# Kernel tuning notes

Measured on AMD Instinct MI355X. Metric: run time of the kernel, lower is better.

## Reference

```python
import jax, jax.numpy as jnp
import numpy as np

N_SUPPORT = 16384
EMBED_DIM = 1024
MAX_LEVELS = 4
N_CLASSES = 64


def setup_inputs() -> dict:
    key = jax.random.key(0)
    ks = jax.random.split(key, 12)
    D, L = EMBED_DIM, MAX_LEVELS
    s = 0.02
    return {
        "support_features": jax.random.normal(ks[0], (N_SUPPORT, D), jnp.float32),
        "support_labels": jax.random.randint(ks[1], (N_SUPPORT,), 0, N_CLASSES),
        "sp_w1": jax.random.normal(ks[2], (D, D // 2), jnp.float32) * s,
        "sp_b1": jnp.zeros((D // 2,), jnp.float32),
        "sp_w2": jax.random.normal(ks[3], (D // 2, L), jnp.float32) * s,
        "sp_b2": jnp.zeros((L,), jnp.float32),
        "lvl_emb": jax.random.normal(ks[4], (L, 1), jnp.float32) * s,
        "an_w1": jax.random.normal(ks[5], (L, D + 1, D), jnp.float32) * s,
        "an_b1": jnp.zeros((L, D), jnp.float32),
        "an_gamma": jnp.ones((L, D), jnp.float32),
        "an_beta": jnp.zeros((L, D), jnp.float32),
        "an_w2": jax.random.normal(ks[6], (L, D, D), jnp.float32) * s,
        "an_b2": jnp.zeros((L, D), jnp.float32),
        "fu_w1": jax.random.normal(ks[7], (L * D + L, D), jnp.float32) * s,
        "fu_b1": jnp.zeros((D,), jnp.float32),
        "fu_w2": jax.random.normal(ks[8], (D, D), jnp.float32) * s,
        "fu_b2": jnp.zeros((D,), jnp.float32),
        "n_classes": N_CLASSES,
    }


def _forward(support_features, support_labels, sp_w1, sp_b1, sp_w2, sp_b2,
             lvl_emb, an_w1, an_b1, an_gamma, an_beta, an_w2, an_b2,
             fu_w1, fu_b1, fu_w2, fu_b2, n_classes):
    N, D = support_features.shape
    L = an_w1.shape[0]
    # structure predictor on task context (mean pooled support set)
    task_context = support_features.mean(axis=0)
    h = jax.nn.relu(task_context @ sp_w1 + sp_b1)
    acts = jax.nn.sigmoid(h @ sp_w2 + sp_b2)  # [L]
    ones = jnp.ones((N,), support_features.dtype)
    counts = jax.ops.segment_sum(ones, support_labels, num_segments=n_classes)[:, None]
    counts = jnp.maximum(counts, 1.0)
    # per-level small MLP over ALL support points, then per-class mean via segment_sum
    protos = []
    for l in range(L):  # fixed small loop over structurally distinct level params
        xl = jnp.concatenate([support_features, jnp.broadcast_to(lvl_emb[l], (N, 1))], axis=1)  # [N, D+1]
        hh = xl @ an_w1[l] + an_b1[l]
        mu = hh.mean(axis=-1, keepdims=True)
        var = ((hh - mu) ** 2).mean(axis=-1, keepdims=True)
        hh = (hh - mu) / jnp.sqrt(var + 1e-5) * an_gamma[l] + an_beta[l]  # LayerNorm eps=1e-5
        hh = jax.nn.relu(hh)
        t = hh @ an_w2[l] + an_b2[l]
        protos.append(jax.ops.segment_sum(t, support_labels, num_segments=n_classes) / counts)
    protos = jnp.stack(protos, axis=1)  # [C, L, D]
    # data-dependent gating: pack prototypes of active levels (act > 0.1) to the front,
    # then active weights, then zero padding -- matching torch's concat+pad layout
    mask = acts > 0.1
    mi = mask.astype(jnp.int32)
    slots = jnp.cumsum(mi) - 1          # destination slot of each active level
    k = mi.sum()                        # number of active levels
    slot_or_dump = jnp.where(mask, slots, L)
    packed = jnp.zeros((n_classes, L + 1, D), protos.dtype).at[:, slot_or_dump, :].set(protos)[:, :L, :]
    S = L * D + L
    buf = jnp.zeros((n_classes, S + 1), protos.dtype)
    buf = buf.at[:, : L * D].set(packed.reshape(n_classes, L * D))
    widx = jnp.where(mask, k * D + slots, S)  # weights placed right after the k packed prototypes
    buf = buf.at[:, widx].set(jnp.broadcast_to(acts, (n_classes, L)))
    fusion_input = buf[:, :S]  # [C, L*D + L]
    fused = jax.nn.relu(fusion_input @ fu_w1 + fu_b1) @ fu_w2 + fu_b2  # [C, D]
    raw_mean = jax.ops.segment_sum(support_features, support_labels, num_segments=n_classes) / counts
    prototypes = jnp.where(k > 0, fused, raw_mean)
    level_contributions = jnp.where(mask, acts, 0.0)
    return prototypes, acts, level_contributions


def reference(support_features, support_labels, sp_w1, sp_b1, sp_w2, sp_b2,
              lvl_emb, an_w1, an_b1, an_gamma, an_beta, an_w2, an_b2,
              fu_w1, fu_b1, fu_w2, fu_b2, n_classes):
    return _forward(support_features, support_labels, sp_w1, sp_b1, sp_w2, sp_b2,
                    lvl_emb, an_w1, an_b1, an_gamma, an_beta, an_w2, an_b2,
                    fu_w1, fu_b1, fu_w2, fu_b2, n_classes)
```

## Files before the change

kernel.cpp:

```cpp
#include <hip/hip_runtime.h>
#include <hip/hip_bf16.h>
#include <stdint.h>

#define N_SUP 16384
#define DIM   1024
#define NLV   4
#define NCLS  64
#define NFUSE 4096

typedef __bf16 bf16x8 __attribute__((ext_vector_type(8)));
typedef __bf16 bf16x4 __attribute__((ext_vector_type(4)));
typedef float  f32x4  __attribute__((ext_vector_type(4)));

#define GLOAD_LDS16(g, l) \
    __builtin_amdgcn_global_load_lds((const __attribute__((address_space(1))) void*)(g), \
                                     (__attribute__((address_space(3))) void*)(l), 16, 0, 0)

__global__ __launch_bounds__(256) void k_count(const int* __restrict__ labels,
                                               int* __restrict__ gcnt) {
    __shared__ int hist[NCLS];
    int tid = threadIdx.x;
    if (tid < NCLS) hist[tid] = 0;
    __syncthreads();
    atomicAdd(&hist[labels[blockIdx.x * 256 + tid]], 1);
    __syncthreads();
    if (tid < NCLS && hist[tid] > 0) atomicAdd(&gcnt[tid], hist[tid]);
}

__global__ __launch_bounds__(64) void k_scan(const int* __restrict__ gcnt,
                                             int* __restrict__ gstart,
                                             int* __restrict__ gcur,
                                             float* __restrict__ counts_f) {
    int tid = threadIdx.x;
    __shared__ int s[NCLS];
    s[tid] = gcnt[tid];
    __syncthreads();
    if (tid == 0) {
        int run = 0;
        for (int c = 0; c < NCLS; ++c) { int v = s[c]; s[c] = run; run += v; }
    }
    __syncthreads();
    gstart[tid] = s[tid];
    gcur[tid] = s[tid];
    counts_f[tid] = fmaxf((float)gcnt[tid], 1.0f);
}

__global__ __launch_bounds__(256) void k_scatter(const int* __restrict__ labels,
                                                 int* __restrict__ gcur,
                                                 int* __restrict__ inv) {
    __shared__ int hist[NCLS];
    __shared__ int base[NCLS];
    int tid = threadIdx.x;
    int r = blockIdx.x * 256 + tid;
    if (tid < NCLS) hist[tid] = 0;
    __syncthreads();
    int lab = labels[r];
    int lrank = atomicAdd(&hist[lab], 1);
    __syncthreads();
    if (tid < NCLS && hist[tid] > 0) base[tid] = atomicAdd(&gcur[tid], hist[tid]);
    __syncthreads();
    inv[r] = base[lab] + lrank;
}

__global__ __launch_bounds__(256) void k_conv_feat(const float* __restrict__ f,
                                                   const int* __restrict__ inv,
                                                   __bf16* __restrict__ o) {
    int r = blockIdx.x;
    int tid = threadIdx.x;
    int dr = inv[r];
    float4 v = *(const float4*)(f + (size_t)r * DIM + tid * 4);
    union { __bf16 b[4]; uint64_t u; } pk;
    pk.b[0] = (__bf16)v.x; pk.b[1] = (__bf16)v.y;
    pk.b[2] = (__bf16)v.z; pk.b[3] = (__bf16)v.w;
    *(uint64_t*)(o + (size_t)dr * DIM + tid * 4) = pk.u;
}

__global__ __launch_bounds__(256) void k_wt(const float* __restrict__ an_w1,
                                            const float* __restrict__ an_b1,
                                            const float* __restrict__ lvl_emb,
                                            __bf16* __restrict__ w1t,
                                            float* __restrict__ eff) {
    __shared__ float tile[64][65];
    int m = blockIdx.z;
    const float* src = an_w1 + (size_t)m * 1025 * 1024;
    __bf16* dst = w1t + (size_t)m * 1024 * 1024;
    int k0 = blockIdx.x * 64, n0 = blockIdx.y * 64;
    int j = threadIdx.x & 63, i0 = threadIdx.x >> 6;
    #pragma unroll
    for (int ii = 0; ii < 16; ++ii) {
        int i = i0 + ii * 4;
        tile[i][j] = src[(size_t)(k0 + i) * 1024 + n0 + j];
    }
    __syncthreads();
    #pragma unroll
    for (int ii = 0; ii < 16; ++ii) {
        int i = i0 + ii * 4;
        dst[(size_t)(n0 + i) * 1024 + k0 + j] = (__bf16)tile[j][i];
    }
    if (blockIdx.y == 0 && threadIdx.x < 64) {
        int jj = k0 + threadIdx.x;
        eff[m * 1024 + jj] = an_b1[m * 1024 + jj]
                           + lvl_emb[m] * src[(size_t)1024 * 1024 + jj];
    }
}

__global__ __launch_bounds__(256) void k_gather(const __bf16* __restrict__ X,
                                                const int* __restrict__ gstart,
                                                const int* __restrict__ gcnt,
                                                float* __restrict__ outp,
                                                float* __restrict__ tcsum) {
    int c = blockIdx.x;
    int col = blockIdx.y * 256 + threadIdx.x;
    int st = gstart[c], n = gcnt[c];
    const __bf16* base = X + (size_t)st * DIM + col;
    float acc = 0.f;
    int i = 0;
    for (; i + 8 <= n; i += 8) {
        float v[8];
        #pragma unroll
        for (int j = 0; j < 8; ++j) v[j] = (float)base[(size_t)(i + j) * DIM];
        #pragma unroll
        for (int j = 0; j < 8; ++j) acc += v[j];
    }
    for (; i < n; ++i) acc += (float)base[(size_t)i * DIM];
    outp[(size_t)c * DIM + col] = acc;
    atomicAdd(&tcsum[col], acc);
}

__global__ __launch_bounds__(512) void k_gemv1(const float* __restrict__ tc,
                                               const float* __restrict__ sp_w1,
                                               float* __restrict__ hpre) {
    __shared__ float tcs[64];
    int tid = threadIdx.x;
    int kb = blockIdx.x * 64;
    if (tid < 64) tcs[tid] = tc[kb + tid] * (1.0f / N_SUP);
    __syncthreads();
    float acc = 0.f;
    #pragma unroll 8
    for (int k = 0; k < 64; ++k)
        acc += tcs[k] * sp_w1[(size_t)(kb + k) * 512 + tid];
    atomicAdd(&hpre[tid], acc);
}

__global__ __launch_bounds__(512) void k_head_fin(const float* __restrict__ hpre,
                                                  const float* __restrict__ sp_b1,
                                                  const float* __restrict__ sp_w2,
                                                  const float* __restrict__ sp_b2,
                                                  float* __restrict__ headf,
                                                  int* __restrict__ headi,
                                                  float* __restrict__ dout) {
    __shared__ float red[512];
    __shared__ float a4[4];
    int tid = threadIdx.x;
    float hv = hpre[tid] + sp_b1[tid];
    hv = hv > 0.f ? hv : 0.f;
    #pragma unroll
    for (int o = 0; o < 4; ++o) {
        red[tid] = hv * sp_w2[tid * 4 + o];
        __syncthreads();
        for (int st = 256; st > 0; st >>= 1) {
            if (tid < st) red[tid] += red[tid + st];
            __syncthreads();
        }
        if (tid == 0) a4[o] = 1.0f / (1.0f + expf(-(red[0] + sp_b2[o])));
        __syncthreads();
    }
    if (tid == 0) {
        int kk = 0;
        int lvl[4] = {-1, -1, -1, -1};
        for (int l = 0; l < 4; ++l)
            if (a4[l] > 0.1f) { lvl[kk] = l; kk++; }
        headi[0] = kk;
        for (int s = 0; s < 4; ++s) headi[1 + s] = lvl[s];
        for (int l = 0; l < 4; ++l) headf[l] = a4[l];
    }
    if (tid < 4) {
        dout[65536 + tid] = a4[tid];
        dout[65540 + tid] = a4[tid] > 0.1f ? a4[tid] : 0.f;
    }
}

__global__ __launch_bounds__(512, 2) void k_gemm256(const __bf16* __restrict__ A,
                                                    const __bf16* __restrict__ Bt,
                                                    const float* __restrict__ bias,
                                                    __bf16* __restrict__ C,
                                                    int K, int Nn, int NT) {
    __shared__ __bf16 lds[65536];
    const int tid = threadIdx.x;
    const int w   = tid >> 6;
    const int l   = tid & 63;
    const int wr  = w >> 2;
    const int wc  = w & 3;
    const int am  = l & 15;
    const int kg  = l >> 4;
    const size_t bm = (size_t)blockIdx.x * 256;
    const size_t bn = (size_t)blockIdx.y * 256;

    const int srow = w * 8 + (l >> 3);
    const int scol = ((l & 7) ^ (l >> 3)) * 8;
    const __bf16* gA[2][2]; const __bf16* gB[2][2];
    #pragma unroll
    for (int h = 0; h < 2; ++h)
        #pragma unroll
        for (int p = 0; p < 2; ++p) {
            gA[h][p] = A  + (bm + h * 128 + p * 64 + srow) * (size_t)K + scol;
            gB[h][p] = Bt + (bn + h * 128 + p * 64 + srow) * (size_t)K + scol;
        }

    f32x4 acc[8][4] = {};
    bf16x8 ax[4][2], ay[4][2], bx[2][2], by[2][2];

    #pragma unroll
    for (int h = 0; h < 2; ++h)
        #pragma unroll
        for (int p = 0; p < 2; ++p) {
            GLOAD_LDS16(gA[h][p], lds + h * 8192 + p * 4096 + w * 512);
            GLOAD_LDS16(gB[h][p], lds + 16384 + h * 8192 + p * 4096 + w * 512);
        }
    asm volatile("s_waitcnt vmcnt(0)" ::: "memory");
    __builtin_amdgcn_s_barrier();

    const int swzr = (am & 7) * 8;
    const int ko0 = (kg * 8) ^ swzr;
    const int ko1 = (32 + kg * 8) ^ swzr;
    {
        const __bf16* pa0 = lds + wr * 8192;
        #pragma unroll
        for (int i = 0; i < 4; ++i) {
            ax[i][0] = *(const bf16x8*)(pa0 + (i * 16 + am) * 64 + ko0);
            ax[i][1] = *(const bf16x8*)(pa0 + (i * 16 + am) * 64 + ko1);
        }
    }

#define MFMAQ(qm, qn, AF, BF) \
    __builtin_amdgcn_s_setprio(1); \
    _Pragma("unroll") \
    for (int i_ = 0; i_ < 4; ++i_) \
        _Pragma("unroll") \
        for (int j_ = 0; j_ < 2; ++j_) \
            _Pragma("unroll") \
            for (int k_ = 0; k_ < 2; ++k_) \
                acc[(qm) * 4 + i_][(qn) * 2 + j_] = __builtin_amdgcn_mfma_f32_16x16x32_bf16( \
                    AF[i_][k_], BF[j_][k_], acc[(qm) * 4 + i_][(qn) * 2 + j_], 0, 0, 0); \
    __builtin_amdgcn_s_setprio(0);

    for (int t = 0; t < NT; ++t) {
        const int cb = (t & 1) * 32768;
        const int nb = cb ^ 32768;
        const int tn = (t + 1) * 64;
        const bool more = (t + 1 < NT);
        const __bf16* pa  = lds + cb + wr * 8192;
        const __bf16* pan = lds + nb + wr * 8192;
        const __bf16* pb  = lds + cb + 16384 + (wc >> 1) * 8192 + (wc & 1) * 4096;

        if (more) {
            GLOAD_LDS16(gA[0][0] + tn, lds + nb + 0 * 4096 + w * 512);
            GLOAD_LDS16(gA[1][0] + tn, lds + nb + 8192 + 0 * 4096 + w * 512);
            asm volatile("s_waitcnt vmcnt(2)" ::: "memory");
        } else {
            asm volatile("s_waitcnt vmcnt(0)" ::: "memory");
        }
        __builtin_amdgcn_s_barrier();
        #pragma unroll
        for (int j = 0; j < 2; ++j) {
            bx[j][0] = *(const bf16x8*)(pb + (j * 16 + am) * 64 + ko0);
            bx[j][1] = *(const bf16x8*)(pb + (j * 16 + am) * 64 + ko1);
        }
        ay[0][0] = *(const bf16x8*)(pa + ((4 + 0) * 16 + am) * 64 + ko0);
        ay[0][1] = *(const bf16x8*)(pa + ((4 + 0) * 16 + am) * 64 + ko1);
        MFMAQ(0, 0, ax, bx)

        if (more) {
            GLOAD_LDS16(gA[0][1] + tn, lds + nb + 1 * 4096 + w * 512);
            GLOAD_LDS16(gA[1][1] + tn, lds + nb + 8192 + 1 * 4096 + w * 512);
        }
        __builtin_amdgcn_s_barrier();
        #pragma unroll
        for (int j = 0; j < 2; ++j) {
            by[j][0] = *(const bf16x8*)(pb + ((2 + j) * 16 + am) * 64 + ko0);
            by[j][1] = *(const bf16x8*)(pb + ((2 + j) * 16 + am) * 64 + ko1);
        }
        ay[1][0] = *(const bf16x8*)(pa + ((4 + 1) * 16 + am) * 64 + ko0);
        ay[1][1] = *(const bf16x8*)(pa + ((4 + 1) * 16 + am) * 64 + ko1);
        MFMAQ(0, 1, ax, by)

        if (more) {
            GLOAD_LDS16(gB[0][0] + tn, lds + nb + 16384 + 0 * 4096 + w * 512);
            GLOAD_LDS16(gB[0][1] + tn, lds + nb + 16384 + 1 * 4096 + w * 512);
            asm volatile("s_waitcnt vmcnt(4)" ::: "memory");
        }
        __builtin_amdgcn_s_barrier();
        #pragma unroll
        for (int i = 2; i < 4; ++i) {
            ay[i][0] = *(const bf16x8*)(pa + ((4 + i) * 16 + am) * 64 + ko0);
            ay[i][1] = *(const bf16x8*)(pa + ((4 + i) * 16 + am) * 64 + ko1);
        }
        if (more) {
            #pragma unroll
            for (int i = 0; i < 2; ++i) {
                ax[i][0] = *(const bf16x8*)(pan + (i * 16 + am) * 64 + ko0);
                ax[i][1] = *(const bf16x8*)(pan + (i * 16 + am) * 64 + ko1);
            }
        }
        MFMAQ(1, 0, ay, bx)

        if (more) {
            GLOAD_LDS16(gB[1][0] + tn, lds + nb + 16384 + 8192 + 0 * 4096 + w * 512);
            GLOAD_LDS16(gB[1][1] + tn, lds + nb + 16384 + 8192 + 1 * 4096 + w * 512);
        }
        __builtin_amdgcn_s_barrier();
        if (more) {
            #pragma unroll
            for (int i = 2; i < 4; ++i) {
                ax[i][0] = *(const bf16x8*)(pan + (i * 16 + am) * 64 + ko0);
                ax[i][1] = *(const bf16x8*)(pan + (i * 16 + am) * 64 + ko1);
            }
        }
        MFMAQ(1, 1, ay, by)
    }
#undef MFMAQ

    const int rbase = kg * 4;
    #pragma unroll
    for (int m = 0; m < 8; ++m) {
        const size_t row = bm + wr * 128 + m * 16 + rbase;
        #pragma unroll
        for (int n = 0; n < 4; ++n) {
            const int col = (int)bn + wc * 64 + n * 16 + am;
            const float bv = bias[col];
            #pragma unroll
            for (int r = 0; r < 4; ++r)
                C[(row + r) * (size_t)Nn + col] = (__bf16)(acc[m][n][r] + bv);
        }
    }
}

__global__ __launch_bounds__(256) void k_gather_ln(const __bf16* __restrict__ hh,
                                                   const float* __restrict__ an_g,
                                                   const float* __restrict__ an_be,
                                                   const int* __restrict__ gstart,
                                                   const int* __restrict__ gcnt,
                                                   float* __restrict__ gsum) {
    int c = blockIdx.x, lv = blockIdx.y, z = blockIdx.z;
    int tid = threadIdx.x;
    int wv = tid >> 6, lane = tid & 63;
    int colb = lane * 16;
    float g[16], b[16];
    #pragma unroll
    for (int j = 0; j < 16; j += 4) {
        float4 gv = *(const float4*)(an_g + lv * 1024 + colb + j);
        float4 bv = *(const float4*)(an_be + lv * 1024 + colb + j);
        g[j] = gv.x; g[j + 1] = gv.y; g[j + 2] = gv.z; g[j + 3] = gv.w;
        b[j] = bv.x; b[j + 1] = bv.y; b[j + 2] = bv.z; b[j + 3] = bv.w;
    }
    int st = gstart[c], n = gcnt[c];
    float acc[16] = {};
    for (int i = z * 4 + wv; i < n; i += 16) {
        const __bf16* row = hh + (size_t)(st + i) * NFUSE + lv * 1024 + colb;
        bf16x8 v0 = *(const bf16x8*)row;
        bf16x8 v1 = *(const bf16x8*)(row + 8);
        float x[16];
        #pragma unroll
        for (int j = 0; j < 8; ++j) { x[j] = (float)v0[j]; x[8 + j] = (float)v1[j]; }
        float s = 0.f, q = 0.f;
        #pragma unroll
        for (int j = 0; j < 16; ++j) { s += x[j]; q += x[j] * x[j]; }
        #pragma unroll
        for (int off = 1; off < 64; off <<= 1) {
            s += __shfl_xor(s, off);
            q += __shfl_xor(q, off);
        }
        float mu = s * (1.0f / DIM);
        float var = q * (1.0f / DIM) - mu * mu;
        float rstd = rsqrtf(var + 1e-5f);
        #pragma unroll
        for (int j = 0; j < 16; ++j) {
            float y = (x[j] - mu) * rstd * g[j] + b[j];
            acc[j] += y > 0.f ? y : 0.f;
        }
    }
    __shared__ float red[4][1024];
    #pragma unroll
    for (int j = 0; j < 16; ++j) red[wv][colb + j] = acc[j];
    __syncthreads();
    for (int col = tid; col < 1024; col += 256) {
        float v = red[0][col] + red[1][col] + red[2][col] + red[3][col];
        atomicAdd(&gsum[(size_t)c * NFUSE + lv * 1024 + col], v);
    }
}

__global__ __launch_bounds__(256) void k_build_fi(const float* __restrict__ proto_pre,
                                                  const float* __restrict__ an_b2,
                                                  const int* __restrict__ gcnt,
                                                  const float* __restrict__ counts_f,
                                                  const float* __restrict__ headf,
                                                  const int* __restrict__ headi,
                                                  float* __restrict__ fi) {
    int idx = blockIdx.x * 256 + threadIdx.x;
    if (idx >= 64 * 4160) return;
    int c = idx / 4160, col = idx % 4160;
    int kk = headi[0];
    float v = 0.f;
    if (col < kk * 1024) {
        int s = col >> 10, d = col & 1023;
        int l = headi[1 + s];
        if (gcnt[c] > 0)
            v = proto_pre[((size_t)l * NCLS + c) * DIM + d] / counts_f[c]
                + an_b2[(size_t)l * DIM + d];
    } else if (col < kk * 1024 + kk) {
        int s = col - kk * 1024;
        v = headf[headi[1 + s]];
    }
    fi[idx] = v;
}

__global__ __launch_bounds__(256) void k_fuse_gemm(const float* __restrict__ Abase, int lda, int az,
                                                   const float* __restrict__ Wbase, int wz,
                                                   float* __restrict__ outbase, int oz,
                                                   const float* __restrict__ abias,
                                                   int K) {
    const float* Afi = Abase + (size_t)blockIdx.z * az;
    const float* W   = Wbase + (size_t)blockIdx.z * wz;
    float* outp      = outbase + (size_t)blockIdx.z * oz;
    __shared__ float fi_lds[64][64];
    int tid = threadIdx.x;
    int tj = tid & 63, tg = tid >> 6;
    int jb = blockIdx.x;
    int k0 = blockIdx.y * 64;
    for (int i = tid; i < 64 * 64; i += 256) {
        int cc = i >> 6, kq = i & 63;
        float av = 0.f;
        if (k0 + kq < lda) {
            av = Afi[(size_t)cc * lda + k0 + kq];
            if (abias) {
                av += abias[k0 + kq];
                av = av > 0.f ? av : 0.f;
            }
        }
        fi_lds[cc][kq] = av;
    }
    __syncthreads();
    float acc[16] = {};
    #pragma unroll 4
    for (int kq = 0; kq < 64; ++kq) {
        int kg = k0 + kq;
        float wv = (kg < K) ? W[(size_t)kg * 1024 + jb * 64 + tj] : 0.f;
        #pragma unroll
        for (int cc = 0; cc < 16; ++cc)
            acc[cc] += fi_lds[tg * 16 + cc][kq] * wv;
    }
    #pragma unroll
    for (int cc = 0; cc < 16; ++cc)
        atomicAdd(&outp[(size_t)(tg * 16 + cc) * 1024 + jb * 64 + tj], acc[cc]);
}

__global__ __launch_bounds__(256) void k_final(const float* __restrict__ pre2,
                                               const float* __restrict__ fu_b2,
                                               const int* __restrict__ headi,
                                               const float* __restrict__ rawsum,
                                               const float* __restrict__ counts_f,
                                               float* __restrict__ dout) {
    int i = blockIdx.x * 256 + threadIdx.x;
    int c = i >> 10, j = i & 1023;
    float v;
    if (headi[0] > 0) v = pre2[i] + fu_b2[j];
    else              v = rawsum[i] / counts_f[c];
    dout[i] = v;
}

extern "C" void kernel_launch(void* const* d_in, const int* in_sizes, int n_in,
                              void* d_out, int out_size, void* d_ws, size_t ws_size,
                              hipStream_t stream) {
    (void)in_sizes; (void)n_in; (void)out_size; (void)ws_size;
    const float* feat    = (const float*)d_in[0];
    const int*   labels  = (const int*)d_in[1];
    const float* sp_w1   = (const float*)d_in[2];
    const float* sp_b1   = (const float*)d_in[3];
    const float* sp_w2   = (const float*)d_in[4];
    const float* sp_b2   = (const float*)d_in[5];
    const float* lvl_emb = (const float*)d_in[6];
    const float* an_w1   = (const float*)d_in[7];
    const float* an_b1   = (const float*)d_in[8];
    const float* an_g    = (const float*)d_in[9];
    const float* an_be   = (const float*)d_in[10];
    const float* an_w2   = (const float*)d_in[11];
    const float* an_b2   = (const float*)d_in[12];
    const float* fu_w1   = (const float*)d_in[13];
    const float* fu_b1   = (const float*)d_in[14];
    const float* fu_w2   = (const float*)d_in[15];
    const float* fu_b2   = (const float*)d_in[16];
    float* dout = (float*)d_out;

    char* p = (char*)d_ws;
    auto alloc = [&](size_t b) { char* r = p; p += (b + 255) & ~(size_t)255; return r; };
    __bf16* featb = (__bf16*)alloc((size_t)N_SUP * DIM * 2);
    __bf16* w1t   = (__bf16*)alloc((size_t)NLV * DIM * DIM * 2);
    __bf16* hh    = (__bf16*)alloc((size_t)N_SUP * NFUSE * 2);
    float*  effb1 = (float*) alloc((size_t)NLV * DIM * 4);
    float*  fi    = (float*) alloc((size_t)64 * 4160 * 4);
    float*  rawsum  = (float*)alloc((size_t)NCLS * DIM * 4);
    int*    inv     = (int*)  alloc((size_t)N_SUP * 4);
    int*    gstart  = (int*)  alloc(NCLS * 4);
    int*    gcur    = (int*)  alloc(NCLS * 4);
    float*  counts_f= (float*)alloc(NCLS * 4);
    float*  headf   = (float*)alloc(4 * 4);
    int*    headi   = (int*)  alloc(8 * 4);
    char* z0 = p;
    int*    gcnt    = (int*)  alloc(NCLS * 4);
    float*  tc      = (float*)alloc(DIM * 4);
    float*  gsum    = (float*)alloc((size_t)NCLS * NFUSE * 4);
    float*  proto_pre = (float*)alloc((size_t)NLV * NCLS * DIM * 4);
    float*  h1pre   = (float*)alloc((size_t)NCLS * DIM * 4);
    float*  f2pre   = (float*)alloc((size_t)NCLS * DIM * 4);
    float*  hpre    = (float*)alloc(512 * 4);
    size_t zbytes = (size_t)(p - z0);
    hipMemsetAsync(z0, 0, zbytes, stream);

    k_count<<<N_SUP / 256, 256, 0, stream>>>(labels, gcnt);
    k_scan<<<1, 64, 0, stream>>>(gcnt, gstart, gcur, counts_f);
    k_scatter<<<N_SUP / 256, 256, 0, stream>>>(labels, gcur, inv);
    k_conv_feat<<<N_SUP, 256, 0, stream>>>(feat, inv, featb);
    k_wt<<<dim3(16, 16, 4), 256, 0, stream>>>(an_w1, an_b1, lvl_emb, w1t, effb1);
    k_gather<<<dim3(NCLS, 4), 256, 0, stream>>>(featb, gstart, gcnt, rawsum, tc);
    k_gemv1<<<16, 512, 0, stream>>>(tc, sp_w1, hpre);
    k_head_fin<<<1, 512, 0, stream>>>(hpre, sp_b1, sp_w2, sp_b2, headf, headi, dout);

    k_gemm256<<<dim3(64, 16), 512, 0, stream>>>(featb, w1t, effb1, hh, DIM, NFUSE, DIM / 64);
    k_gather_ln<<<dim3(NCLS, NLV, 4), 256, 0, stream>>>(hh, an_g, an_be, gstart, gcnt, gsum);
    k_fuse_gemm<<<dim3(16, 16, 4), 256, 0, stream>>>(gsum, NFUSE, 1024,
                                                     an_w2, 1024 * 1024,
                                                     proto_pre, NCLS * DIM, nullptr, 1024);

    k_build_fi<<<(64 * 4160) / 256, 256, 0, stream>>>(proto_pre, an_b2, gcnt, counts_f,
                                                      headf, headi, fi);
    k_fuse_gemm<<<dim3(16, 65, 1), 256, 0, stream>>>(fi, 4160, 0, fu_w1, 0,
                                                     h1pre, 0, nullptr, 4100);
    k_fuse_gemm<<<dim3(16, 16, 1), 256, 0, stream>>>(h1pre, 1024, 0, fu_w2, 0,
                                                     f2pre, 0, fu_b1, 1024);
    k_final<<<NCLS * DIM / 256, 256, 0, stream>>>(f2pre, fu_b2, headi, rawsum, counts_f, dout);
}
```

Before: 313.9 us.

## Merge prep kernels and piggyback head MLP onto GEMM launches

Merges feature conversion, weight transpose and raw class-sum gather into one launch. The gather now reads the original fp32 features through a new row list, so it no longer depends on the converted bf16 buffer. The task-context GEMV becomes extra blocks in the big GEMM launch, and the head finalisation becomes an extra z-slice of the first fuse GEMM. This cuts the kernel launch count and serialization gaps. The cost is larger fp32 random-row reads in the gather and some branch and LDS overhead in the merged kernels.

After: 331.5 us. 5.6% more time.

```diff
diff --git a/kernel.cpp b/kernel.cpp
--- a/kernel.cpp
+++ b/kernel.cpp
@@ -47,7 +47,8 @@
 
 __global__ __launch_bounds__(256) void k_scatter(const int* __restrict__ labels,
                                                  int* __restrict__ gcur,
-                                                 int* __restrict__ inv) {
+                                                 int* __restrict__ inv,
+                                                 int* __restrict__ rowlist) {
     __shared__ int hist[NCLS];
     __shared__ int base[NCLS];
     int tid = threadIdx.x;
@@ -59,124 +60,79 @@
     __syncthreads();
     if (tid < NCLS && hist[tid] > 0) base[tid] = atomicAdd(&gcur[tid], hist[tid]);
     __syncthreads();
-    inv[r] = base[lab] + lrank;
-}
-
-__global__ __launch_bounds__(256) void k_conv_feat(const float* __restrict__ f,
-                                                   const int* __restrict__ inv,
-                                                   __bf16* __restrict__ o) {
-    int r = blockIdx.x;
-    int tid = threadIdx.x;
-    int dr = inv[r];
-    float4 v = *(const float4*)(f + (size_t)r * DIM + tid * 4);
-    union { __bf16 b[4]; uint64_t u; } pk;
-    pk.b[0] = (__bf16)v.x; pk.b[1] = (__bf16)v.y;
-    pk.b[2] = (__bf16)v.z; pk.b[3] = (__bf16)v.w;
-    *(uint64_t*)(o + (size_t)dr * DIM + tid * 4) = pk.u;
-}
-
-__global__ __launch_bounds__(256) void k_wt(const float* __restrict__ an_w1,
-                                            const float* __restrict__ an_b1,
-                                            const float* __restrict__ lvl_emb,
-                                            __bf16* __restrict__ w1t,
-                                            float* __restrict__ eff) {
+    int pos = base[lab] + lrank;
+    inv[r] = pos;
+    rowlist[pos] = r;
+}
+
+__global__ __launch_bounds__(256) void k_prep(const float* __restrict__ feat,
+                                              const int* __restrict__ inv,
+                                              const int* __restrict__ rowlist,
+                                              const float* __restrict__ an_w1,
+                                              const float* __restrict__ an_b1,
+                                              const float* __restrict__ lvl_emb,
+                                              const int* __restrict__ gstart,
+                                              const int* __restrict__ gcnt,
+                                              __bf16* __restrict__ featb,
+                                              __bf16* __restrict__ w1t,
+                                              float* __restrict__ eff,
+                                              float* __restrict__ rawsum,
+                                              float* __restrict__ tcsum) {
     __shared__ float tile[64][65];
-    int m = blockIdx.z;
-    const float* src = an_w1 + (size_t)m * 1025 * 1024;
-    __bf16* dst = w1t + (size_t)m * 1024 * 1024;
-    int k0 = blockIdx.x * 64, n0 = blockIdx.y * 64;
-    int j = threadIdx.x & 63, i0 = threadIdx.x >> 6;
-    #pragma unroll
-    for (int ii = 0; ii < 16; ++ii) {
-        int i = i0 + ii * 4;
-        tile[i][j] = src[(size_t)(k0 + i) * 1024 + n0 + j];
-    }
-    __syncthreads();
-    #pragma unroll
-    for (int ii = 0; ii < 16; ++ii) {
-        int i = i0 + ii * 4;
-        dst[(size_t)(n0 + i) * 1024 + k0 + j] = (__bf16)tile[j][i];
-    }
-    if (blockIdx.y == 0 && threadIdx.x < 64) {
-        int jj = k0 + threadIdx.x;
-        eff[m * 1024 + jj] = an_b1[m * 1024 + jj]
-                           + lvl_emb[m] * src[(size_t)1024 * 1024 + jj];
-    }
-}
-
-__global__ __launch_bounds__(256) void k_gather(const __bf16* __restrict__ X,
-                                                const int* __restrict__ gstart,
-                                                const int* __restrict__ gcnt,
-                                                float* __restrict__ outp,
-                                                float* __restrict__ tcsum) {
-    int c = blockIdx.x;
-    int col = blockIdx.y * 256 + threadIdx.x;
-    int st = gstart[c], n = gcnt[c];
-    const __bf16* base = X + (size_t)st * DIM + col;
-    float acc = 0.f;
-    int i = 0;
-    for (; i + 8 <= n; i += 8) {
-        float v[8];
-        #pragma unroll
-        for (int j = 0; j < 8; ++j) v[j] = (float)base[(size_t)(i + j) * DIM];
-        #pragma unroll
-        for (int j = 0; j < 8; ++j) acc += v[j];
-    }
-    for (; i < n; ++i) acc += (float)base[(size_t)i * DIM];
-    outp[(size_t)c * DIM + col] = acc;
-    atomicAdd(&tcsum[col], acc);
-}
-
-__global__ __launch_bounds__(512) void k_gemv1(const float* __restrict__ tc,
-                                               const float* __restrict__ sp_w1,
-                                               float* __restrict__ hpre) {
-    __shared__ float tcs[64];
-    int tid = threadIdx.x;
-    int kb = blockIdx.x * 64;
-    if (tid < 64) tcs[tid] = tc[kb + tid] * (1.0f / N_SUP);
-    __syncthreads();
-    float acc = 0.f;
-    #pragma unroll 8
-    for (int k = 0; k < 64; ++k)
-        acc += tcs[k] * sp_w1[(size_t)(kb + k) * 512 + tid];
-    atomicAdd(&hpre[tid], acc);
-}
-
-__global__ __launch_bounds__(512) void k_head_fin(const float* __restrict__ hpre,
-                                                  const float* __restrict__ sp_b1,
-                                                  const float* __restrict__ sp_w2,
-                                                  const float* __restrict__ sp_b2,
-                                                  float* __restrict__ headf,
-                                                  int* __restrict__ headi,
-                                                  float* __restrict__ dout) {
-    __shared__ float red[512];
-    __shared__ float a4[4];
-    int tid = threadIdx.x;
-    float hv = hpre[tid] + sp_b1[tid];
-    hv = hv > 0.f ? hv : 0.f;
-    #pragma unroll
-    for (int o = 0; o < 4; ++o) {
-        red[tid] = hv * sp_w2[tid * 4 + o];
+    const int lin = blockIdx.x;
+    const int tid = threadIdx.x;
+    if (lin < 16384) {
+        int r = lin;
+        int dr = inv[r];
+        float4 v = *(const float4*)(feat + (size_t)r * DIM + tid * 4);
+        union { __bf16 b[4]; uint64_t u; } pk;
+        pk.b[0] = (__bf16)v.x; pk.b[1] = (__bf16)v.y;
+        pk.b[2] = (__bf16)v.z; pk.b[3] = (__bf16)v.w;
+        *(uint64_t*)(featb + (size_t)dr * DIM + tid * 4) = pk.u;
+    } else if (lin < 16384 + 1024) {
+        int idx = lin - 16384;
+        int m = idx >> 8;
+        int rem = idx & 255;
+        int k0 = (rem & 15) * 64, n0 = (rem >> 4) * 64;
+        const float* src = an_w1 + (size_t)m * 1025 * 1024;
+        __bf16* dst = w1t + (size_t)m * 1024 * 1024;
+        int j = tid & 63, i0 = tid >> 6;
+        #pragma unroll
+        for (int ii = 0; ii < 16; ++ii) {
+            int i = i0 + ii * 4;
+            tile[i][j] = src[(size_t)(k0 + i) * 1024 + n0 + j];
+        }
         __syncthreads();
-        for (int st = 256; st > 0; st >>= 1) {
-            if (tid < st) red[tid] += red[tid + st];
-            __syncthreads();
-        }
-        if (tid == 0) a4[o] = 1.0f / (1.0f + expf(-(red[0] + sp_b2[o])));
-        __syncthreads();
-    }
-    if (tid == 0) {
-        int kk = 0;
-        int lvl[4] = {-1, -1, -1, -1};
-        for (int l = 0; l < 4; ++l)
-            if (a4[l] > 0.1f) { lvl[kk] = l; kk++; }
-        headi[0] = kk;
-        for (int s = 0; s < 4; ++s) headi[1 + s] = lvl[s];
-        for (int l = 0; l < 4; ++l) headf[l] = a4[l];
-    }
-    if (tid < 4) {
-        dout[65536 + tid] = a4[tid];
-        dout[65540 + tid] = a4[tid] > 0.1f ? a4[tid] : 0.f;
+        #pragma unroll
+        for (int ii = 0; ii < 16; ++ii) {
+            int i = i0 + ii * 4;
+            dst[(size_t)(n0 + i) * 1024 + k0 + j] = (__bf16)tile[j][i];
+        }
+        if ((rem >> 4) == 0 && tid < 64) {
+            int jj = k0 + tid;
+            eff[m * 1024 + jj] = an_b1[m * 1024 + jj]
+                               + lvl_emb[m] * src[(size_t)1024 * 1024 + jj];
+        }
+    } else {
+        int idx = lin - 17408;
+        int c = idx >> 2;
+        int col = (idx & 3) * 256 + tid;
+        int st = gstart[c], n = gcnt[c];
+        float acc = 0.f;
+        int i = 0;
+        for (; i + 8 <= n; i += 8) {
+            int r[8];
+            #pragma unroll
+            for (int j = 0; j < 8; ++j) r[j] = rowlist[st + i + j];
+            float v[8];
+            #pragma unroll
+            for (int j = 0; j < 8; ++j) v[j] = feat[(size_t)r[j] * DIM + col];
+            #pragma unroll
+            for (int j = 0; j < 8; ++j) acc += v[j];
+        }
+        for (; i < n; ++i) acc += feat[(size_t)rowlist[st + i] * DIM + col];
+        rawsum[(size_t)c * DIM + col] = acc;
+        atomicAdd(&tcsum[col], acc);
     }
 }
 
@@ -184,7 +140,24 @@
                                                     const __bf16* __restrict__ Bt,
                                                     const float* __restrict__ bias,
                                                     __bf16* __restrict__ C,
+                                                    const float* __restrict__ tc,
+                                                    const float* __restrict__ sp_w1,
+                                                    float* __restrict__ hpre,
                                                     int K, int Nn, int NT) {
+    const int lin = blockIdx.x;
+    if (lin >= 1024) {
+        __shared__ float tcs[64];
+        int tid = threadIdx.x;
+        int kb = (lin - 1024) * 64;
+        if (tid < 64) tcs[tid] = tc[kb + tid] * (1.0f / N_SUP);
+        __syncthreads();
+        float acc = 0.f;
+        #pragma unroll 8
+        for (int k = 0; k < 64; ++k)
+            acc += tcs[k] * sp_w1[(size_t)(kb + k) * 512 + tid];
+        atomicAdd(&hpre[tid], acc);
+        return;
+    }
     __shared__ __bf16 lds[65536];
     const int tid = threadIdx.x;
     const int w   = tid >> 6;
@@ -193,8 +166,8 @@
     const int wc  = w & 3;
     const int am  = l & 15;
     const int kg  = l >> 4;
-    const size_t bm = (size_t)blockIdx.x * 256;
-    const size_t bn = (size_t)blockIdx.y * 256;
+    const size_t bm = (size_t)(lin & 63) * 256;
+    const size_t bn = (size_t)(lin >> 6) * 256;
 
     const int srow = w * 8 + (l >> 3);
     const int scol = ((l & 7) ^ (l >> 3)) * 8;
@@ -418,7 +391,49 @@
                                                    const float* __restrict__ Wbase, int wz,
                                                    float* __restrict__ outbase, int oz,
                                                    const float* __restrict__ abias,
-                                                   int K) {
+                                                   int K, int do_head,
+                                                   const float* __restrict__ hpre,
+                                                   const float* __restrict__ sp_b1,
+                                                   const float* __restrict__ sp_w2,
+                                                   const float* __restrict__ sp_b2,
+                                                   float* __restrict__ headf,
+                                                   int* __restrict__ headi,
+                                                   float* __restrict__ dout) {
+    if (do_head && blockIdx.z == 4) {
+        if (blockIdx.x != 0 || blockIdx.y != 0) return;
+        __shared__ float hred[256];
+        __shared__ float ha4[4];
+        int tid = threadIdx.x;
+        float hv0 = hpre[tid] + sp_b1[tid];
+        hv0 = hv0 > 0.f ? hv0 : 0.f;
+        float hv1 = hpre[tid + 256] + sp_b1[tid + 256];
+        hv1 = hv1 > 0.f ? hv1 : 0.f;
+        #pragma unroll
+        for (int o = 0; o < 4; ++o) {
+            hred[tid] = hv0 * sp_w2[tid * 4 + o] + hv1 * sp_w2[(tid + 256) * 4 + o];
+            __syncthreads();
+            for (int st = 128; st > 0; st >>= 1) {
+                if (tid < st) hred[tid] += hred[tid + st];
+                __syncthreads();
+            }
+            if (tid == 0) ha4[o] = 1.0f / (1.0f + expf(-(hred[0] + sp_b2[o])));
+            __syncthreads();
+        }
+        if (tid == 0) {
+            int kk = 0;
+            int lvl[4] = {-1, -1, -1, -1};
+            for (int l = 0; l < 4; ++l)
+                if (ha4[l] > 0.1f) { lvl[kk] = l; kk++; }
+            headi[0] = kk;
+            for (int s = 0; s < 4; ++s) headi[1 + s] = lvl[s];
+            for (int l = 0; l < 4; ++l) headf[l] = ha4[l];
+        }
+        if (tid < 4) {
+            dout[65536 + tid] = ha4[tid];
+            dout[65540 + tid] = ha4[tid] > 0.1f ? ha4[tid] : 0.f;
+        }
+        return;
+    }
     const float* Afi = Abase + (size_t)blockIdx.z * az;
     const float* W   = Wbase + (size_t)blockIdx.z * wz;
     float* outp      = outbase + (size_t)blockIdx.z * oz;
@@ -500,6 +515,7 @@
     float*  fi    = (float*) alloc((size_t)64 * 4160 * 4);
     float*  rawsum  = (float*)alloc((size_t)NCLS * DIM * 4);
     int*    inv     = (int*)  alloc((size_t)N_SUP * 4);
+    int*    rowlist = (int*)  alloc((size_t)N_SUP * 4);
     int*    gstart  = (int*)  alloc(NCLS * 4);
     int*    gcur    = (int*)  alloc(NCLS * 4);
     float*  counts_f= (float*)alloc(NCLS * 4);
@@ -518,24 +534,27 @@
 
     k_count<<<N_SUP / 256, 256, 0, stream>>>(labels, gcnt);
     k_scan<<<1, 64, 0, stream>>>(gcnt, gstart, gcur, counts_f);
-    k_scatter<<<N_SUP / 256, 256, 0, stream>>>(labels, gcur, inv);
-    k_conv_feat<<<N_SUP, 256, 0, stream>>>(feat, inv, featb);
-    k_wt<<<dim3(16, 16, 4), 256, 0, stream>>>(an_w1, an_b1, lvl_emb, w1t, effb1);
-    k_gather<<<dim3(NCLS, 4), 256, 0, stream>>>(featb, gstart, gcnt, rawsum, tc);
-    k_gemv1<<<16, 512, 0, stream>>>(tc, sp_w1, hpre);
-    k_head_fin<<<1, 512, 0, stream>>>(hpre, sp_b1, sp_w2, sp_b2, headf, headi, dout);
-
-    k_gemm256<<<dim3(64, 16), 512, 0, stream>>>(featb, w1t, effb1, hh, DIM, NFUSE, DIM / 64);
+    k_scatter<<<N_SUP / 256, 256, 0, stream>>>(labels, gcur, inv, rowlist);
+    k_prep<<<16384 + 1024 + 256, 256, 0, stream>>>(feat, inv, rowlist, an_w1, an_b1,
+                                                   lvl_emb, gstart, gcnt,
+                                                   featb, w1t, effb1, rawsum, tc);
+    k_gemm256<<<1024 + 16, 512, 0, stream>>>(featb, w1t, effb1, hh,
+                                             tc, sp_w1, hpre, DIM, NFUSE, DIM / 64);
     k_gather_ln<<<dim3(NCLS, NLV, 4), 256, 0, stream>>>(hh, an_g, an_be, gstart, gcnt, gsum);
-    k_fuse_gemm<<<dim3(16, 16, 4), 256, 0, stream>>>(gsum, NFUSE, 1024,
+    k_fuse_gemm<<<dim3(16, 16, 5), 256, 0, stream>>>(gsum, NFUSE, 1024,
                                                      an_w2, 1024 * 1024,
-                                                     proto_pre, NCLS * DIM, nullptr, 1024);
-
+                                                     proto_pre, NCLS * DIM, nullptr, 1024,
+                                                     1, hpre, sp_b1, sp_w2, sp_b2,
+                                                     headf, headi, dout);
     k_build_fi<<<(64 * 4160) / 256, 256, 0, stream>>>(proto_pre, an_b2, gcnt, counts_f,
                                                       headf, headi, fi);
     k_fuse_gemm<<<dim3(16, 65, 1), 256, 0, stream>>>(fi, 4160, 0, fu_w1, 0,
-                                                     h1pre, 0, nullptr, 4100);
+                                                     h1pre, 0, nullptr, 4100,
+                                                     0, nullptr, nullptr, nullptr, nullptr,
+                                                     nullptr, nullptr, nullptr);
     k_fuse_gemm<<<dim3(16, 16, 1), 256, 0, stream>>>(h1pre, 1024, 0, fu_w2, 0,
-                                                     f2pre, 0, fu_b1, 1024);
+                                                     f2pre, 0, fu_b1, 1024,
+                                                     0, nullptr, nullptr, nullptr, nullptr,
+                                                     nullptr, nullptr, nullptr);
     k_final<<<NCLS * DIM / 256, 256, 0, stream>>>(f2pre, fu_b2, headi, rawsum, counts_f, dout);
 }
```
